# Performance work log

Measured on AMD Instinct MI355X. Metric: run time of the kernel, lower is better.

## Reference

```python
import jax, jax.numpy as jnp
import numpy as np

N = 4_194_304   # samples per polarization
L = 513         # impulse response taps


def setup_inputs() -> dict:
    key = jax.random.key(0)
    k1, k2, k3, k4 = jax.random.split(key, 4)
    tx_real = jax.random.normal(k1, (2, N), dtype=jnp.float32)
    tx_imag = jax.random.normal(k2, (2, N), dtype=jnp.float32)
    h_real = jax.random.normal(k3, (L,), dtype=jnp.float32)
    h_imag = jax.random.normal(k4, (L,), dtype=jnp.float32)
    return {"tx_real": tx_real, "tx_imag": tx_imag, "h_real": h_real, "h_imag": h_imag}


def reference(tx_real, tx_imag, h_real, h_imag):
    # Dual-pol complex baseband signal [2, N]; same taps h [L] applied to each pol.
    tx = tx_real + 1j * tx_imag          # complex64 [2, N]
    h = h_real + 1j * h_imag             # complex64 [L]
    n_out = tx.shape[-1] + h.shape[0] - 1  # 'full' convolution length
    # FFT-based full convolution, both polarizations batched in one FFT call
    # (mathematically identical to overlap-save convolution in 'full' mode).
    X = jnp.fft.fft(tx, n=n_out, axis=-1)   # [2, n_out]
    H = jnp.fft.fft(h, n=n_out)             # [n_out]
    y = jnp.fft.ifft(X * H[None, :], axis=-1)  # [2, n_out] complex
    # Return real/imag stacked so the output is a real array: [2, n_out, 2]
    return jnp.stack([y.real, y.imag], axis=-1)
```

## Files before the change

### kernel.cpp

```cpp
#include <hip/hip_runtime.h>
#include <hip/hip_bf16.h>


#define NSAMP 4194304
#define LTAPS 513
#define NOUT  (NSAMP + LTAPS - 1)

#define BLK       256
#define WAVES     4
#define MR        8
#define TILE_OUT  256
#define WAVE_OUT  (MR * TILE_OUT)
#define BLOCK_OUT (WAVES * WAVE_OUT)
#define HALO      512
#define XELEMS    (BLOCK_OUT + HALO + 16)
#define NB        17

__device__ __forceinline__ int xswz(int e) { return e + ((e >> 6) << 3); }
#define XSZ 9808

#define HROWS 552
__device__ __forceinline__ int hswz(int R) { return (R << 3) + ((R >> 3) << 3); }
#define HSZ 4968

typedef __attribute__((ext_vector_type(8))) short short8;
typedef __attribute__((ext_vector_type(4))) short short4v;
typedef __attribute__((ext_vector_type(4))) float float4v;

__device__ __forceinline__ short f2b(float f) {
    __bf16 b = (__bf16)f;
    return __builtin_bit_cast(short, b);
}

__global__ __launch_bounds__(BLK, 2)
void fir_mfma(const float* __restrict__ txr_all, const float* __restrict__ txi_all,
              const float* __restrict__ hr_g, const float* __restrict__ hi_g,
              float2* __restrict__ out) {
    const int pol = blockIdx.y;
    const long long N0 = (long long)blockIdx.x * BLOCK_OUT;
    const int tid = threadIdx.x;

    __shared__ short xr_s[XSZ];
    __shared__ short xi_s[XSZ];
    __shared__ short hr_s[HSZ];
    __shared__ short hi_s[HSZ];
    __shared__ short nhi_s[HSZ];

    const float* __restrict__ xr_g = txr_all + (size_t)pol * NSAMP;
    const float* __restrict__ xi_g = txi_all + (size_t)pol * NSAMP;

    #pragma unroll
    for (int it = 0; it < 9; ++it) {
        int e = (tid + it * BLK) * 4;
        if (e < XELEMS) {
            long long g = N0 - HALO + e;
            float r0, r1, r2, r3, i0, i1, i2, i3;
            if (g >= 0 && g + 3 < NSAMP) {
                float4 fr = *(const float4*)(xr_g + g);
                float4 fi = *(const float4*)(xi_g + g);
                r0 = fr.x; r1 = fr.y; r2 = fr.z; r3 = fr.w;
                i0 = fi.x; i1 = fi.y; i2 = fi.z; i3 = fi.w;
            } else {
                long long gc0 = min(max(g + 0, 0LL), (long long)NSAMP - 1);
                long long gc1 = min(max(g + 1, 0LL), (long long)NSAMP - 1);
                long long gc2 = min(max(g + 2, 0LL), (long long)NSAMP - 1);
                long long gc3 = min(max(g + 3, 0LL), (long long)NSAMP - 1);
                r0 = (g + 0 >= 0 && g + 0 < NSAMP) ? xr_g[gc0] : 0.0f;
                r1 = (g + 1 >= 0 && g + 1 < NSAMP) ? xr_g[gc1] : 0.0f;
                r2 = (g + 2 >= 0 && g + 2 < NSAMP) ? xr_g[gc2] : 0.0f;
                r3 = (g + 3 >= 0 && g + 3 < NSAMP) ? xr_g[gc3] : 0.0f;
                i0 = (g + 0 >= 0 && g + 0 < NSAMP) ? xi_g[gc0] : 0.0f;
                i1 = (g + 1 >= 0 && g + 1 < NSAMP) ? xi_g[gc1] : 0.0f;
                i2 = (g + 2 >= 0 && g + 2 < NSAMP) ? xi_g[gc2] : 0.0f;
                i3 = (g + 3 >= 0 && g + 3 < NSAMP) ? xi_g[gc3] : 0.0f;
            }
            int ls = xswz(e);
            short4v vr = { f2b(r0), f2b(r1), f2b(r2), f2b(r3) };
            short4v vi = { f2b(i0), f2b(i1), f2b(i2), f2b(i3) };
            *(short4v*)(xr_s + ls) = vr;
            *(short4v*)(xi_s + ls) = vi;
        }
    }

    #pragma unroll
    for (int it = 0; it < 3; ++it) {
        int R = tid + it * BLK;
        if (R < HROWS) {
            short8 vr, vi, vni;
            #pragma unroll
            for (int t = 0; t < 8; ++t) {
                int idx = R - 24 - t;
                float fr = (idx >= 0 && idx < LTAPS) ? hr_g[idx] : 0.0f;
                float fi = (idx >= 0 && idx < LTAPS) ? hi_g[idx] : 0.0f;
                vr[t] = f2b(fr);
                vi[t] = f2b(fi);
                vni[t] = f2b(-fi);
            }
            int hs = hswz(R);
            *(short8*)(hr_s + hs) = vr;
            *(short8*)(hi_s + hs) = vi;
            *(short8*)(nhi_s + hs) = vni;
        }
    }

    __syncthreads();

    const int lane = tid & 63;
    const int wave = tid >> 6;
    const int c = lane & 15;
    const int q = lane >> 4;

    float4v acc_re[MR], acc_im[MR];
    #pragma unroll
    for (int m = 0; m < MR; ++m) {
        acc_re[m] = (float4v){0.f, 0.f, 0.f, 0.f};
        acc_im[m] = (float4v){0.f, 0.f, 0.f, 0.f};
    }

    for (int b = 0; b < NB; ++b) {
        int Rh = 32 * b + c - 8 * q + 24;
        int hs = hswz(Rh);
        short8 fhr  = *(const short8*)(hr_s + hs);
        short8 fhi  = *(const short8*)(hi_s + hs);
        short8 fnhi = *(const short8*)(nhi_s + hs);
        int ebase = HALO + wave * WAVE_OUT + 16 * c + 8 * q - 32 * b;
        #pragma unroll
        for (int m = 0; m < MR; ++m) {
            int ls = xswz(ebase + m * TILE_OUT);
            short8 fxr = *(const short8*)(xr_s + ls);
            short8 fxi = *(const short8*)(xi_s + ls);
            acc_re[m] = __builtin_amdgcn_mfma_f32_16x16x32_bf16(fxr, fhr,  acc_re[m], 0, 0, 0);
            acc_re[m] = __builtin_amdgcn_mfma_f32_16x16x32_bf16(fxi, fnhi, acc_re[m], 0, 0, 0);
            acc_im[m] = __builtin_amdgcn_mfma_f32_16x16x32_bf16(fxr, fhi,  acc_im[m], 0, 0, 0);
            acc_im[m] = __builtin_amdgcn_mfma_f32_16x16x32_bf16(fxi, fhr,  acc_im[m], 0, 0, 0);
        }
    }

    float2* __restrict__ op = out + (size_t)pol * NOUT;
    const long long nwave = N0 + (long long)wave * WAVE_OUT;
    #pragma unroll
    for (int m = 0; m < MR; ++m) {
        #pragma unroll
        for (int v = 0; v < 4; ++v) {
            int rrow = q * 4 + v;
            long long n = nwave + m * TILE_OUT + 16 * rrow + c;
            if (n < NOUT) op[n] = make_float2(acc_re[m][v], acc_im[m][v]);
        }
    }
}

extern "C" void kernel_launch(void* const* d_in, const int* in_sizes, int n_in,
                              void* d_out, int out_size, void* d_ws, size_t ws_size,
                              hipStream_t stream) {
    const float* txr = (const float*)d_in[0];
    const float* txi = (const float*)d_in[1];
    const float* hr  = (const float*)d_in[2];
    const float* hi  = (const float*)d_in[3];
    float2* out = (float2*)d_out;

    const int blocks_per_pol = (NOUT + BLOCK_OUT - 1) / BLOCK_OUT;
    dim3 grid(blocks_per_pol, 2);
    fir_mfma<<<grid, BLK, 0, stream>>>(txr, txi, hr, hi, out);
}
```

Before: 165.8 us.

## Switch FIR to 32x32x16 MFMA with taps prebuilt in global workspace

Replaces the 16x16x32 bf16 MFMA tiling with 32x32x16 MFMAs: each wave computes a 1024-output tile over 34 tap blocks, and block size shrinks to 4096 outputs. The Toeplitz tap matrix (real, imag, negated imag) is now built once by a separate kernel into the workspace and read from global/L2 instead of being rebuilt in LDS by every block. LDS drops to the input signal only, and launch bounds allow more blocks per CU to raise occupancy. The cost is more per-block halo overhead, per-iteration global loads of the taps, and an extra kernel launch.

```diff
diff --git a/kernel.cpp b/kernel.cpp
--- a/kernel.cpp
+++ b/kernel.cpp
@@ -8,52 +8,66 @@
 
 #define BLK       256
 #define WAVES     4
-#define MR        8
-#define TILE_OUT  256
-#define WAVE_OUT  (MR * TILE_OUT)
-#define BLOCK_OUT (WAVES * WAVE_OUT)
+#define WAVE_OUT  1024
+#define BLOCK_OUT 4096
 #define HALO      512
 #define XELEMS    (BLOCK_OUT + HALO + 16)
-#define NB        17
+#define NB        34
+#define HROWS     568
+#define NBLK      ((NOUT + BLOCK_OUT - 1) / BLOCK_OUT)
 
-__device__ __forceinline__ int xswz(int e) { return e + ((e >> 6) << 3); }
-#define XSZ 9808
+typedef __attribute__((ext_vector_type(8)))  short short8;
+typedef __attribute__((ext_vector_type(4)))  short short4v;
+typedef __attribute__((ext_vector_type(16))) float float16v;
 
-#define HROWS 552
-__device__ __forceinline__ int hswz(int R) { return (R << 3) + ((R >> 3) << 3); }
-#define HSZ 4968
-
-typedef __attribute__((ext_vector_type(8))) short short8;
-typedef __attribute__((ext_vector_type(4))) short short4v;
-typedef __attribute__((ext_vector_type(4))) float float4v;
+__device__ __forceinline__ int xswz(int e) { return e + ((e >> 5) << 3); }
+#define XSZ 5776
 
 __device__ __forceinline__ short f2b(float f) {
     __bf16 b = (__bf16)f;
     return __builtin_bit_cast(short, b);
 }
 
-__global__ __launch_bounds__(BLK, 2)
-void fir_mfma(const float* __restrict__ txr_all, const float* __restrict__ txi_all,
-              const float* __restrict__ hr_g, const float* __restrict__ hi_g,
-              float2* __restrict__ out) {
+__global__ __launch_bounds__(BLK)
+void build_h(const float* __restrict__ hr, const float* __restrict__ hi,
+             short* __restrict__ hh) {
+    int R = blockIdx.x * BLK + threadIdx.x;
+    if (R < HROWS) {
+        short8 vr, vi, vn;
+        #pragma unroll
+        for (int j = 0; j < 8; ++j) {
+            int idx = R - 24 - j;
+            bool ok = (idx >= 0) && (idx < LTAPS);
+            float fr = ok ? hr[idx] : 0.0f;
+            float fi = ok ? hi[idx] : 0.0f;
+            vr[j] = f2b(fr);
+            vi[j] = f2b(fi);
+            vn[j] = f2b(-fi);
+        }
+        *(short8*)(hh + (size_t)(0 * HROWS + R) * 8) = vr;
+        *(short8*)(hh + (size_t)(1 * HROWS + R) * 8) = vi;
+        *(short8*)(hh + (size_t)(2 * HROWS + R) * 8) = vn;
+    }
+}
+
+__global__ __launch_bounds__(BLK, 4)
+void fir_mfma32(const float* __restrict__ txr_all, const float* __restrict__ txi_all,
+                const short* __restrict__ hh, float2* __restrict__ out) {
     const int pol = blockIdx.y;
-    const long long N0 = (long long)blockIdx.x * BLOCK_OUT;
+    const int N0  = blockIdx.x * BLOCK_OUT;
     const int tid = threadIdx.x;
 
     __shared__ short xr_s[XSZ];
     __shared__ short xi_s[XSZ];
-    __shared__ short hr_s[HSZ];
-    __shared__ short hi_s[HSZ];
-    __shared__ short nhi_s[HSZ];
 
     const float* __restrict__ xr_g = txr_all + (size_t)pol * NSAMP;
     const float* __restrict__ xi_g = txi_all + (size_t)pol * NSAMP;
 
     #pragma unroll
-    for (int it = 0; it < 9; ++it) {
+    for (int it = 0; it < 5; ++it) {
         int e = (tid + it * BLK) * 4;
         if (e < XELEMS) {
-            long long g = N0 - HALO + e;
+            int g = N0 - HALO + e;
             float r0, r1, r2, r3, i0, i1, i2, i3;
             if (g >= 0 && g + 3 < NSAMP) {
                 float4 fr = *(const float4*)(xr_g + g);
@@ -61,10 +75,10 @@
                 r0 = fr.x; r1 = fr.y; r2 = fr.z; r3 = fr.w;
                 i0 = fi.x; i1 = fi.y; i2 = fi.z; i3 = fi.w;
             } else {
-                long long gc0 = min(max(g + 0, 0LL), (long long)NSAMP - 1);
-                long long gc1 = min(max(g + 1, 0LL), (long long)NSAMP - 1);
-                long long gc2 = min(max(g + 2, 0LL), (long long)NSAMP - 1);
-                long long gc3 = min(max(g + 3, 0LL), (long long)NSAMP - 1);
+                int gc0 = min(max(g + 0, 0), NSAMP - 1);
+                int gc1 = min(max(g + 1, 0), NSAMP - 1);
+                int gc2 = min(max(g + 2, 0), NSAMP - 1);
+                int gc3 = min(max(g + 3, 0), NSAMP - 1);
                 r0 = (g + 0 >= 0 && g + 0 < NSAMP) ? xr_g[gc0] : 0.0f;
                 r1 = (g + 1 >= 0 && g + 1 < NSAMP) ? xr_g[gc1] : 0.0f;
                 r2 = (g + 2 >= 0 && g + 2 < NSAMP) ? xr_g[gc2] : 0.0f;
@@ -81,71 +95,40 @@
             *(short4v*)(xi_s + ls) = vi;
         }
     }
-
-    #pragma unroll
-    for (int it = 0; it < 3; ++it) {
-        int R = tid + it * BLK;
-        if (R < HROWS) {
-            short8 vr, vi, vni;
-            #pragma unroll
-            for (int t = 0; t < 8; ++t) {
-                int idx = R - 24 - t;
-                float fr = (idx >= 0 && idx < LTAPS) ? hr_g[idx] : 0.0f;
-                float fi = (idx >= 0 && idx < LTAPS) ? hi_g[idx] : 0.0f;
-                vr[t] = f2b(fr);
-                vi[t] = f2b(fi);
-                vni[t] = f2b(-fi);
-            }
-            int hs = hswz(R);
-            *(short8*)(hr_s + hs) = vr;
-            *(short8*)(hi_s + hs) = vi;
-            *(short8*)(nhi_s + hs) = vni;
-        }
-    }
-
     __syncthreads();
 
     const int lane = tid & 63;
     const int wave = tid >> 6;
-    const int c = lane & 15;
-    const int q = lane >> 4;
+    const int cc   = lane & 31;
+    const int half = lane >> 5;
 
-    float4v acc_re[MR], acc_im[MR];
-    #pragma unroll
-    for (int m = 0; m < MR; ++m) {
-        acc_re[m] = (float4v){0.f, 0.f, 0.f, 0.f};
-        acc_im[m] = (float4v){0.f, 0.f, 0.f, 0.f};
-    }
+    float16v acc_re = {0.f,0.f,0.f,0.f,0.f,0.f,0.f,0.f,0.f,0.f,0.f,0.f,0.f,0.f,0.f,0.f};
+    float16v acc_im = {0.f,0.f,0.f,0.f,0.f,0.f,0.f,0.f,0.f,0.f,0.f,0.f,0.f,0.f,0.f,0.f};
+
+    const int   ebase = HALO + wave * WAVE_OUT + 32 * cc + 8 * half + 16;
+    const short* hp0  = hh + (size_t)(cc - 8 * half + 8) * 8;
 
     for (int b = 0; b < NB; ++b) {
-        int Rh = 32 * b + c - 8 * q + 24;
-        int hs = hswz(Rh);
-        short8 fhr  = *(const short8*)(hr_s + hs);
-        short8 fhi  = *(const short8*)(hi_s + hs);
-        short8 fnhi = *(const short8*)(nhi_s + hs);
-        int ebase = HALO + wave * WAVE_OUT + 16 * c + 8 * q - 32 * b;
-        #pragma unroll
-        for (int m = 0; m < MR; ++m) {
-            int ls = xswz(ebase + m * TILE_OUT);
-            short8 fxr = *(const short8*)(xr_s + ls);
-            short8 fxi = *(const short8*)(xi_s + ls);
-            acc_re[m] = __builtin_amdgcn_mfma_f32_16x16x32_bf16(fxr, fhr,  acc_re[m], 0, 0, 0);
-            acc_re[m] = __builtin_amdgcn_mfma_f32_16x16x32_bf16(fxi, fnhi, acc_re[m], 0, 0, 0);
-            acc_im[m] = __builtin_amdgcn_mfma_f32_16x16x32_bf16(fxr, fhi,  acc_im[m], 0, 0, 0);
-            acc_im[m] = __builtin_amdgcn_mfma_f32_16x16x32_bf16(fxi, fhr,  acc_im[m], 0, 0, 0);
-        }
+        const short* hp = hp0 + (size_t)(16 * b) * 8;
+        short8 fhr = *(const short8*)(hp);
+        short8 fhi = *(const short8*)(hp + (size_t)HROWS * 8);
+        short8 fnh = *(const short8*)(hp + (size_t)(2 * HROWS) * 8);
+        int ls = xswz(ebase - 16 * b);
+        short8 fxr = *(const short8*)(xr_s + ls);
+        short8 fxi = *(const short8*)(xi_s + ls);
+        acc_re = __builtin_amdgcn_mfma_f32_32x32x16_bf16(fxr, fhr, acc_re, 0, 0, 0);
+        acc_re = __builtin_amdgcn_mfma_f32_32x32x16_bf16(fxi, fnh, acc_re, 0, 0, 0);
+        acc_im = __builtin_amdgcn_mfma_f32_32x32x16_bf16(fxr, fhi, acc_im, 0, 0, 0);
+        acc_im = __builtin_amdgcn_mfma_f32_32x32x16_bf16(fxi, fhr, acc_im, 0, 0, 0);
     }
 
     float2* __restrict__ op = out + (size_t)pol * NOUT;
-    const long long nwave = N0 + (long long)wave * WAVE_OUT;
+    const int nw = N0 + wave * WAVE_OUT;
     #pragma unroll
-    for (int m = 0; m < MR; ++m) {
-        #pragma unroll
-        for (int v = 0; v < 4; ++v) {
-            int rrow = q * 4 + v;
-            long long n = nwave + m * TILE_OUT + 16 * rrow + c;
-            if (n < NOUT) op[n] = make_float2(acc_re[m][v], acc_im[m][v]);
-        }
+    for (int v = 0; v < 16; ++v) {
+        int row = (v & 3) + 8 * (v >> 2) + 4 * half;
+        int n = nw + 32 * row + cc;
+        if (n < NOUT) op[n] = make_float2(acc_re[v], acc_im[v]);
     }
 }
 
@@ -157,8 +140,10 @@
     const float* hr  = (const float*)d_in[2];
     const float* hi  = (const float*)d_in[3];
     float2* out = (float2*)d_out;
+    short* hh = (short*)d_ws;
 
-    const int blocks_per_pol = (NOUT + BLOCK_OUT - 1) / BLOCK_OUT;
-    dim3 grid(blocks_per_pol, 2);
-    fir_mfma<<<grid, BLK, 0, stream>>>(txr, txi, hr, hi, out);
+    build_h<<<dim3((HROWS + BLK - 1) / BLK), BLK, 0, stream>>>(hr, hi, hh);
+
+    dim3 grid(NBLK, 2);
+    fir_mfma32<<<grid, BLK, 0, stream>>>(txr, txi, hh, out);
 }
```

After: 147.2 us. 1.13x faster.
